# Performance work log

Hardware: AMD Instinct MI355X
Metric: run time of the kernel (lower is better)

The kernel has to match this reference:

```python
import jax, jax.numpy as jnp
import numpy as np

B, C, LH, LW = 2, 64, 64, 64
KSIZE = 3
HO, WO = LH * 4, LW * 4          # fold output size
HR, WR = HO - KSIZE + 1, WO - KSIZE + 1  # ref spatial size so unfold L == fold L


def setup_inputs() -> dict:
    key = jax.random.key(0)
    k1, k2, k3 = jax.random.split(key, 3)
    lr = jax.random.normal(k1, (B, C, LH, LW), dtype=jnp.float32)
    ref = jax.random.normal(k2, (B, C, HR, WR), dtype=jnp.float32)
    L = HR * WR
    index_map = jax.random.randint(k3, (B, L), 0, L)
    return {"lr": lr, "ref": ref, "index_map": index_map}


def reference(lr, ref, index_map):
    b, c, lh, lw = lr.shape
    k = KSIZE
    ho, wo = lh * 4, lw * 4
    hr, wr = ref.shape[2], ref.shape[3]
    # 'same' padding for ksize=3, stride=1, rate=1 -> reflect pad 1 on each side
    padded = jnp.pad(ref, ((0, 0), (0, 0), (1, 1), (1, 1)), mode='reflect')
    # im2col / unfold, torch channel ordering (C, kh, kw): [B, C, k, k, hr, wr]
    patches = jnp.stack(
        [jnp.stack([padded[:, :, i:i + hr, j:j + wr] for j in range(k)], axis=2)
         for i in range(k)], axis=2)
    patches = patches.reshape(b, c * k * k, hr * wr)  # [B, C*k*k, L]
    # indexed gather along the patch (L) dimension
    idx = jnp.broadcast_to(index_map[:, None, :], patches.shape)
    warped = jnp.take_along_axis(patches, idx, axis=2)
    # col2im / fold with overlap-add to (ho, wo), kernel k, stride 1, pad 0
    hb, wb = ho - k + 1, wo - k + 1  # == hr, wr
    p = warped.reshape(b, c, k, k, hb, wb)
    out = jnp.zeros((b, c, ho, wo), dtype=ref.dtype)
    for i in range(k):
        for j in range(k):
            out = out.at[:, :, i:i + hb, j:j + wb].add(p[:, :, i, j])
    return out
```

## Files before the change

### kernel.cpp

```cpp
#include <hip/hip_runtime.h>
#include <hip/hip_fp16.h>


#define B_   2
#define C_   64
#define HR_  254
#define WR_  254
#define HO_  256
#define WO_  256
#define L_   (HR_ * WR_)
#define PLANE_ (HO_ * WO_ * C_)

__global__ __launch_bounds__(256) void pad_transpose_h_kernel(
    const float* __restrict__ ref, _Float16* __restrict__ P)
{
    __shared__ float srow[C_][255];

    unsigned bid = blockIdx.x;
    unsigned b  = bid >> 8;
    unsigned py = bid & 255u;
    int ry = (py == 0) ? 1 : ((py == HO_ - 1) ? HR_ - 2 : (int)py - 1);

    const float* rrow = ref + ((size_t)b * C_) * (HR_ * WR_) + (size_t)ry * WR_;
    unsigned tid = threadIdx.x;
    for (unsigned e = tid; e < C_ * WR_; e += 256) {
        unsigned c = e / WR_;
        unsigned w = e - c * WR_;
        srow[c][w] = rrow[(size_t)c * (HR_ * WR_) + w];
    }
    __syncthreads();

    unsigned cpair = tid & 31u;
    unsigned wv    = tid >> 5;
    _Float16* prow = P + ((size_t)(b * HO_ + py) * WO_) * C_;
    for (unsigned k = 0; k < WO_ / 8; ++k) {
        unsigned px = k * 8 + wv;
        int rx = (px == 0) ? 1 : ((px == WO_ - 1) ? WR_ - 2 : (int)px - 1);
        _Float16 h0 = (_Float16)srow[2 * cpair][rx];
        _Float16 h1 = (_Float16)srow[2 * cpair + 1][rx];
        union { _Float16 h[2]; unsigned u; } pk;
        pk.h[0] = h0; pk.h[1] = h1;
        *reinterpret_cast<unsigned*>(prow + (size_t)px * C_ + 2 * cpair) = pk.u;
    }
}

__global__ __launch_bounds__(256) void warp_gather3_kernel(
    const _Float16* __restrict__ P,
    const int*      __restrict__ index_map,
    float*          __restrict__ out)
{
    __shared__ unsigned sbase[3][66];
    __shared__ float    slds[64][65];

    unsigned p  = blockIdx.x;
    unsigned wg = (p & 7u) * 256u + (p >> 3);
    unsigned b    = wg >> 10;
    unsigned rest = wg & 1023u;
    unsigned y    = rest >> 2;
    unsigned x0   = (rest & 3u) * 64u;
    unsigned tid  = threadIdx.x;

    const int* imb = index_map + (size_t)b * L_;
    if (tid < 3 * 66) {
        unsigned r    = tid / 66;
        unsigned ccol = tid - r * 66;
        int ly = (int)y - 2 + (int)r;
        int lx = (int)(x0 + ccol) - 2;
        unsigned v = 0xFFFFFFFFu;
        if (ly >= 0 && ly < HR_ && lx >= 0 && lx < WR_) {
            unsigned src = (unsigned)imb[ly * WR_ + lx];
            unsigned sy  = src / WR_;
            unsigned sx  = src - sy * WR_;
            v = (sy * (unsigned)WO_ + sx) * (unsigned)C_;
        }
        sbase[r][ccol] = v;
    }
    __syncthreads();

    unsigned wv   = tid >> 6;
    unsigned lane = tid & 63u;
    unsigned q    = lane >> 3;
    unsigned cg   = lane & 7u;
    const _Float16* Pp = P + (size_t)b * PLANE_;

    #pragma unroll
    for (unsigned t = 0; t < 2; ++t) {
        unsigned pxl = wv * 16u + t * 8u + q;

        uint4 raw[9];
        float msk[9];
        #pragma unroll
        for (int k = 0; k < 9; ++k) {
            int i = k / 3, j = k % 3;
            unsigned v = sbase[2 - i][pxl + 2u - (unsigned)j];
            bool valid = (v != 0xFFFFFFFFu);
            unsigned off = (valid ? v : 0u)
                         + (unsigned)((i * WO_ + j) * C_) + cg * 8u;
            msk[k] = valid ? 1.0f : 0.0f;
            raw[k] = *reinterpret_cast<const uint4*>(Pp + off);
        }

        float acc[8] = {0.f, 0.f, 0.f, 0.f, 0.f, 0.f, 0.f, 0.f};
        #pragma unroll
        for (int k = 0; k < 9; ++k) {
            union { uint4 u; _Float16 h[8]; } cv;
            cv.u = raw[k];
            #pragma unroll
            for (int m = 0; m < 8; ++m) {
                acc[m] = fmaf((float)cv.h[m], msk[k], acc[m]);
            }
        }
        *reinterpret_cast<float4*>(&slds[pxl][cg * 8u]) =
            make_float4(acc[0], acc[1], acc[2], acc[3]);
        *reinterpret_cast<float4*>(&slds[pxl][cg * 8u + 4u]) =
            make_float4(acc[4], acc[5], acc[6], acc[7]);
    }
    __syncthreads();

    float* ob = out + ((size_t)b * C_) * (HO_ * WO_) + (size_t)y * WO_ + x0;
    #pragma unroll
    for (unsigned s = 0; s < 16; ++s) {
        unsigned ch = wv * 16u + s;
        ob[(size_t)ch * (HO_ * WO_) + lane] = slds[lane][ch];
    }
}

extern "C" void kernel_launch(void* const* d_in, const int* in_sizes, int n_in,
                              void* d_out, int out_size, void* d_ws, size_t ws_size,
                              hipStream_t stream) {
    const float* ref       = (const float*)d_in[1];
    const int*   index_map = (const int*)d_in[2];
    float*       out       = (float*)d_out;

    _Float16* P = (_Float16*)d_ws;
    pad_transpose_h_kernel<<<dim3(B_ * HO_), dim3(256), 0, stream>>>(ref, P);
    warp_gather3_kernel<<<dim3(B_ * HO_ * 4), dim3(256), 0, stream>>>(P, index_map, out);
}
```

Measured before the change: 36.90 us.

## Split pad-transpose and gather kernels into finer tiles with fp16 staging

The pad/transpose kernel now handles 64-pixel column tiles per block (4x more blocks), converting to fp16 before staging in shared memory and writing packed channel pairs. The gather kernel halves its tile to 32 output pixels per block, so each thread processes one pixel instead of two. It also drops the XCD-swizzled block ordering and uses nontemporal stores for the output. The aim is more blocks for better occupancy and latency hiding. In exchange, less work is amortized per block and index_map halo reads are duplicated across more tiles.

```diff
diff --git a/kernel.cpp b/kernel.cpp
--- a/kernel.cpp
+++ b/kernel.cpp
@@ -11,59 +11,64 @@
 #define L_   (HR_ * WR_)
 #define PLANE_ (HO_ * WO_ * C_)
 
-__global__ __launch_bounds__(256) void pad_transpose_h_kernel(
+__global__ __launch_bounds__(256) void pad_transpose_h2(
     const float* __restrict__ ref, _Float16* __restrict__ P)
 {
-    __shared__ float srow[C_][255];
+    __shared__ unsigned short srow[C_][66];
 
-    unsigned bid = blockIdx.x;
-    unsigned b  = bid >> 8;
-    unsigned py = bid & 255u;
+    unsigned bid  = blockIdx.x;
+    unsigned b    = bid >> 10;
+    unsigned rest = bid & 1023u;
+    unsigned py   = rest >> 2;
+    unsigned x0   = (rest & 3u) * 64u;
     int ry = (py == 0) ? 1 : ((py == HO_ - 1) ? HR_ - 2 : (int)py - 1);
 
     const float* rrow = ref + ((size_t)b * C_) * (HR_ * WR_) + (size_t)ry * WR_;
     unsigned tid = threadIdx.x;
-    for (unsigned e = tid; e < C_ * WR_; e += 256) {
-        unsigned c = e / WR_;
-        unsigned w = e - c * WR_;
-        srow[c][w] = rrow[(size_t)c * (HR_ * WR_) + w];
+
+    #pragma unroll
+    for (unsigned k = 0; k < 16; ++k) {
+        unsigned e = k * 256u + tid;
+        unsigned c = e >> 6, u = e & 63u;
+        unsigned px = x0 + u;
+        int rx = (px == 0) ? 1 : ((px == WO_ - 1) ? WR_ - 2 : (int)px - 1);
+        float v = rrow[(size_t)c * (HR_ * WR_) + rx];
+        _Float16 h = (_Float16)v;
+        srow[c][u] = __builtin_bit_cast(unsigned short, h);
     }
     __syncthreads();
 
-    unsigned cpair = tid & 31u;
-    unsigned wv    = tid >> 5;
-    _Float16* prow = P + ((size_t)(b * HO_ + py) * WO_) * C_;
-    for (unsigned k = 0; k < WO_ / 8; ++k) {
-        unsigned px = k * 8 + wv;
-        int rx = (px == 0) ? 1 : ((px == WO_ - 1) ? WR_ - 2 : (int)px - 1);
-        _Float16 h0 = (_Float16)srow[2 * cpair][rx];
-        _Float16 h1 = (_Float16)srow[2 * cpair + 1][rx];
-        union { _Float16 h[2]; unsigned u; } pk;
-        pk.h[0] = h0; pk.h[1] = h1;
-        *reinterpret_cast<unsigned*>(prow + (size_t)px * C_ + 2 * cpair) = pk.u;
+    _Float16* prow = P + ((size_t)(b * HO_ + py) * WO_ + x0) * C_;
+    #pragma unroll
+    for (unsigned it = 0; it < 8; ++it) {
+        unsigned u2  = it * 256u + tid;
+        unsigned cp  = u2 & 31u;
+        unsigned pxl = u2 >> 5;
+        unsigned pk = (unsigned)srow[2 * cp][pxl]
+                    | ((unsigned)srow[2 * cp + 1][pxl] << 16);
+        *reinterpret_cast<unsigned*>(prow + (size_t)pxl * C_ + 2 * cp) = pk;
     }
 }
 
-__global__ __launch_bounds__(256) void warp_gather3_kernel(
+__global__ __launch_bounds__(256) void warp_gather4_kernel(
     const _Float16* __restrict__ P,
     const int*      __restrict__ index_map,
     float*          __restrict__ out)
 {
-    __shared__ unsigned sbase[3][66];
-    __shared__ float    slds[64][65];
+    __shared__ unsigned sbase[3][36];
+    __shared__ float    slds[32][65];
 
-    unsigned p  = blockIdx.x;
-    unsigned wg = (p & 7u) * 256u + (p >> 3);
-    unsigned b    = wg >> 10;
-    unsigned rest = wg & 1023u;
-    unsigned y    = rest >> 2;
-    unsigned x0   = (rest & 3u) * 64u;
+    unsigned bid  = blockIdx.x;
+    unsigned b    = bid >> 11;
+    unsigned rest = bid & 2047u;
+    unsigned y    = rest >> 3;
+    unsigned x0   = (rest & 7u) * 32u;
     unsigned tid  = threadIdx.x;
 
     const int* imb = index_map + (size_t)b * L_;
-    if (tid < 3 * 66) {
-        unsigned r    = tid / 66;
-        unsigned ccol = tid - r * 66;
+    if (tid < 108) {
+        unsigned r    = tid / 36;
+        unsigned ccol = tid - r * 36;
         int ly = (int)y - 2 + (int)r;
         int lx = (int)(x0 + ccol) - 2;
         unsigned v = 0xFFFFFFFFu;
@@ -81,47 +86,46 @@
     unsigned lane = tid & 63u;
     unsigned q    = lane >> 3;
     unsigned cg   = lane & 7u;
+    unsigned pxl  = wv * 8u + q;
     const _Float16* Pp = P + (size_t)b * PLANE_;
 
+    uint4 raw[9];
+    float msk[9];
     #pragma unroll
-    for (unsigned t = 0; t < 2; ++t) {
-        unsigned pxl = wv * 16u + t * 8u + q;
+    for (int k = 0; k < 9; ++k) {
+        int i = k / 3, j = k % 3;
+        unsigned v = sbase[2 - i][pxl + 2u - (unsigned)j];
+        bool valid = (v != 0xFFFFFFFFu);
+        unsigned off = (valid ? v : 0u)
+                     + (unsigned)((i * WO_ + j) * C_) + cg * 8u;
+        msk[k] = valid ? 1.0f : 0.0f;
+        raw[k] = *reinterpret_cast<const uint4*>(Pp + off);
+    }
 
-        uint4 raw[9];
-        float msk[9];
+    float acc[8] = {0.f, 0.f, 0.f, 0.f, 0.f, 0.f, 0.f, 0.f};
+    #pragma unroll
+    for (int k = 0; k < 9; ++k) {
+        union { uint4 u; _Float16 h[8]; } cv;
+        cv.u = raw[k];
         #pragma unroll
-        for (int k = 0; k < 9; ++k) {
-            int i = k / 3, j = k % 3;
-            unsigned v = sbase[2 - i][pxl + 2u - (unsigned)j];
-            bool valid = (v != 0xFFFFFFFFu);
-            unsigned off = (valid ? v : 0u)
-                         + (unsigned)((i * WO_ + j) * C_) + cg * 8u;
-            msk[k] = valid ? 1.0f : 0.0f;
-            raw[k] = *reinterpret_cast<const uint4*>(Pp + off);
+        for (int m = 0; m < 8; ++m) {
+            acc[m] = fmaf((float)cv.h[m], msk[k], acc[m]);
         }
-
-        float acc[8] = {0.f, 0.f, 0.f, 0.f, 0.f, 0.f, 0.f, 0.f};
-        #pragma unroll
-        for (int k = 0; k < 9; ++k) {
-            union { uint4 u; _Float16 h[8]; } cv;
-            cv.u = raw[k];
-            #pragma unroll
-            for (int m = 0; m < 8; ++m) {
-                acc[m] = fmaf((float)cv.h[m], msk[k], acc[m]);
-            }
-        }
-        *reinterpret_cast<float4*>(&slds[pxl][cg * 8u]) =
-            make_float4(acc[0], acc[1], acc[2], acc[3]);
-        *reinterpret_cast<float4*>(&slds[pxl][cg * 8u + 4u]) =
-            make_float4(acc[4], acc[5], acc[6], acc[7]);
     }
+    *reinterpret_cast<float4*>(&slds[pxl][cg * 8u]) =
+        make_float4(acc[0], acc[1], acc[2], acc[3]);
+    *reinterpret_cast<float4*>(&slds[pxl][cg * 8u + 4u]) =
+        make_float4(acc[4], acc[5], acc[6], acc[7]);
     __syncthreads();
 
     float* ob = out + ((size_t)b * C_) * (HO_ * WO_) + (size_t)y * WO_ + x0;
     #pragma unroll
-    for (unsigned s = 0; s < 16; ++s) {
-        unsigned ch = wv * 16u + s;
-        ob[(size_t)ch * (HO_ * WO_) + lane] = slds[lane][ch];
+    for (unsigned it = 0; it < 8; ++it) {
+        unsigned u2 = it * 256u + tid;
+        unsigned px = u2 & 31u;
+        unsigned ch = u2 >> 5;
+        __builtin_nontemporal_store(slds[px][ch],
+                                    ob + (size_t)ch * (HO_ * WO_) + px);
     }
 }
 
@@ -133,6 +137,6 @@
     float*       out       = (float*)d_out;
 
     _Float16* P = (_Float16*)d_ws;
-    pad_transpose_h_kernel<<<dim3(B_ * HO_), dim3(256), 0, stream>>>(ref, P);
-    warp_gather3_kernel<<<dim3(B_ * HO_ * 4), dim3(256), 0, stream>>>(P, index_map, out);
+    pad_transpose_h2<<<dim3(B_ * HO_ * 4), dim3(256), 0, stream>>>(ref, P);
+    warp_gather4_kernel<<<dim3(B_ * HO_ * 8), dim3(256), 0, stream>>>(P, index_map, out);
 }
```

Result: faster. 36.01 us (-2.4%).
